# Kernel tuning notes

Hardware: AMD Instinct MI355X
Metric: run time of the kernel (lower is better)

## Reference

```python
import jax, jax.numpy as jnp
import numpy as np

N_EMBD = 1024
N_HEAD = 16
T_LEN = 4096
BATCH = 1


def setup_inputs() -> dict:
    key = jax.random.key(0)
    ks = jax.random.split(key, 9)
    C = N_EMBD
    s = 1.0 / np.sqrt(C)
    inp = {
        "x": jax.random.normal(ks[0], (BATCH, T_LEN, C), dtype=jnp.float32),
        "wq": jax.random.normal(ks[1], (C, C), dtype=jnp.float32) * s,
        "bq": jax.random.normal(ks[2], (C,), dtype=jnp.float32) * s,
        "wk": jax.random.normal(ks[3], (C, C), dtype=jnp.float32) * s,
        "bk": jax.random.normal(ks[4], (C,), dtype=jnp.float32) * s,
        "wv": jax.random.normal(ks[5], (C, C), dtype=jnp.float32) * s,
        "bv": jax.random.normal(ks[6], (C,), dtype=jnp.float32) * s,
        "wp": jax.random.normal(ks[7], (C, C), dtype=jnp.float32) * s,
        "bp": jax.random.normal(ks[8], (C,), dtype=jnp.float32) * s,
    }
    return inp


def reference(x, wq, bq, wk, bk, wv, bv, wp, bp):
    B, T, C = x.shape
    H = N_HEAD
    D = C // H  # head_dim
    # torch nn.Linear: y = x @ W.T + b
    def lin(x, w, b):
        return jnp.einsum("btc,oc->bto", x, w) + b
    q = lin(x, wq, bq).reshape(B, T, H, D).transpose(0, 2, 1, 3)  # bhtd
    k = lin(x, wk, bk).reshape(B, T, H, D).transpose(0, 2, 1, 3)
    v = lin(x, wv, bv).reshape(B, T, H, D).transpose(0, 2, 1, 3)
    att = jnp.einsum("bhqd,bhkd->bhqk", q, k) / jnp.sqrt(jnp.float32(D))
    causal = jnp.tril(jnp.ones((T, T), dtype=bool))  # [T,T]
    att = jnp.where(causal[None, None, :, :], att, -jnp.inf)
    att = jax.nn.softmax(att, axis=-1)
    # dropout p=0.0 -> identity (eval equivalent)
    y = jnp.einsum("bhqk,bhkd->bhqd", att, v)
    y = y.transpose(0, 2, 1, 3).reshape(B, T, C)
    return jnp.einsum("btc,oc->bto", y, wp) + bp
```

## Files before the change

kernel.cpp:

```cpp
#include <hip/hip_runtime.h>
#include <stdint.h>

#define T_LEN 4096
#define C_DIM 1024
#define NH 16
#define CLOG2E 0.18033688011112042f

typedef uint16_t u16;
typedef __attribute__((ext_vector_type(4))) float f32x4;
typedef __attribute__((ext_vector_type(8))) __bf16 bf16x8;
typedef __attribute__((ext_vector_type(8))) uint16_t u16x8;
typedef __attribute__((ext_vector_type(4))) float fvec4;

static __device__ __forceinline__ u16 f2b(float f) {
  union { float f; uint32_t u; } v; v.f = f;
  uint32_t u = v.u;
  return (u16)((u + 0x7fffu + ((u >> 16) & 1u)) >> 16);
}

static __device__ __forceinline__ float b2f(u16 b) {
  union { uint32_t u; float f; } v; v.u = ((uint32_t)b) << 16;
  return v.f;
}

static __device__ __forceinline__ uint32_t cvtpk(float lo, float hi) {
  uint32_t r;
  asm("v_cvt_pk_bf16_f32 %0, %1, %2" : "=v"(r) : "v"(lo), "v"(hi));
  return r;
}

static __device__ __forceinline__ f32x4 mfma16(u16x8 a, u16x8 b, f32x4 c) {
  return __builtin_amdgcn_mfma_f32_16x16x32_bf16(
      __builtin_bit_cast(bf16x8, a), __builtin_bit_cast(bf16x8, b), c, 0, 0, 0);
}

static __device__ __forceinline__ void gload_lds16(const void* g, void* l) {
  __builtin_amdgcn_global_load_lds(
      (const __attribute__((address_space(1))) uint32_t*)g,
      (__attribute__((address_space(3))) uint32_t*)l, 16, 0, 0);
}

__global__ void cast_all(const float* __restrict__ x,
                         const float* __restrict__ wq, const float* __restrict__ wk,
                         const float* __restrict__ wv, const float* __restrict__ wp,
                         u16* __restrict__ xb,
                         u16* __restrict__ wqb, u16* __restrict__ wkb,
                         u16* __restrict__ wvb, u16* __restrict__ wpb) {
  int i = blockIdx.x * blockDim.x + threadIdx.x;
  if (i >= 131072) return;
  const int z = blockIdx.y;
  const float* in;
  u16* out;
  if (z < 4) {
    in  = (z == 0) ? wq  : (z == 1) ? wk  : (z == 2) ? wv  : wp;
    out = (z == 0) ? wqb : (z == 1) ? wkb : (z == 2) ? wvb : wpb;
  } else {
    in  = x  + (size_t)(z - 4) * 131072 * 8;
    out = xb + (size_t)(z - 4) * 131072 * 8;
  }
  const fvec4* p = (const fvec4*)(in + (size_t)i * 8);
  fvec4 a = p[0], b = p[1];
  u16x8 o;
  o[0] = f2b(a[0]); o[1] = f2b(a[1]); o[2] = f2b(a[2]); o[3] = f2b(a[3]);
  o[4] = f2b(b[0]); o[5] = f2b(b[1]); o[6] = f2b(b[2]); o[7] = f2b(b[3]);
  *(u16x8*)(out + (size_t)i * 8) = o;
}

__global__ __launch_bounds__(256) void gemm_qkv(
    const u16* __restrict__ xb,
    const u16* __restrict__ wqb, const u16* __restrict__ wkb, const u16* __restrict__ wvb,
    const float* __restrict__ bq, const float* __restrict__ bk, const float* __restrict__ bv,
    u16* __restrict__ qh, u16* __restrict__ kh, u16* __restrict__ vt)
{
  __shared__ u16 sA[128 * 32];
  __shared__ u16 sB[128 * 32];
  const int K = C_DIM;
  const int z = blockIdx.z;
  const u16* wb = (z == 0) ? wqb : (z == 1) ? wkb : wvb;
  const float* bias = (z == 0) ? bq : (z == 1) ? bk : bv;
  const int m0 = blockIdx.x * 128;
  const int n0 = blockIdx.y * 128;
  const int tid = threadIdx.x;
  const int lane = tid & 63;
  const int w = tid >> 6;
  const int wm = (w >> 1) * 64;
  const int wn = (w & 1) * 64;
  const int lr = lane & 15;
  const int lk = (lane >> 4) * 8;

  f32x4 acc[4][4];
#pragma unroll
  for (int m = 0; m < 4; ++m)
#pragma unroll
    for (int n = 0; n < 4; ++n) acc[m][n] = (f32x4){0.f, 0.f, 0.f, 0.f};

  const int srow = tid >> 2;
  const int scol = (tid & 3) * 8;
  const u16* gA = xb + (size_t)(m0 + srow) * K + scol;
  const u16* gB = wb + (size_t)(n0 + srow) * K + scol;

  for (int k0 = 0; k0 < K; k0 += 32) {
    gload_lds16(gA + k0,          &sA[tid * 8]);
    gload_lds16(gA + 64 * K + k0, &sA[2048 + tid * 8]);
    gload_lds16(gB + k0,          &sB[tid * 8]);
    gload_lds16(gB + 64 * K + k0, &sB[2048 + tid * 8]);
    __syncthreads();
    u16x8 af[4], bfr[4];
#pragma unroll
    for (int m = 0; m < 4; ++m) af[m]  = *(const u16x8*)&sA[(wm + m * 16 + lr) * 32 + lk];
#pragma unroll
    for (int n = 0; n < 4; ++n) bfr[n] = *(const u16x8*)&sB[(wn + n * 16 + lr) * 32 + lk];
#pragma unroll
    for (int m = 0; m < 4; ++m)
#pragma unroll
      for (int n = 0; n < 4; ++n) acc[m][n] = mfma16(af[m], bfr[n], acc[m][n]);
    __syncthreads();
  }

  const int lg = lane >> 4;
#pragma unroll
  for (int n = 0; n < 4; ++n) {
    const int o = n0 + wn + n * 16 + lr;
    const float bb = bias[o];
    const int h = o >> 6;
    const int d = o & 63;
#pragma unroll
    for (int m = 0; m < 4; ++m) {
      const int tb = m0 + wm + m * 16 + lg * 4;
      if (z == 2) {
        uint2 pk;
        pk.x = cvtpk(acc[m][n][0] + bb, acc[m][n][1] + bb);
        pk.y = cvtpk(acc[m][n][2] + bb, acc[m][n][3] + bb);
        *(uint2*)&vt[(size_t)o * T_LEN + tb] = pk;
      } else if (z == 0) {
#pragma unroll
        for (int r = 0; r < 4; ++r)
          qh[((size_t)h * T_LEN + tb + r) * 64 + d] = f2b((acc[m][n][r] + bb) * CLOG2E);
      } else {
#pragma unroll
        for (int r = 0; r < 4; ++r)
          kh[((size_t)h * T_LEN + tb + r) * 64 + d] = f2b(acc[m][n][r] + bb);
      }
    }
  }
}

__global__ __launch_bounds__(256) void gemm_proj(
    const u16* __restrict__ yb, const u16* __restrict__ wpb,
    const float* __restrict__ bp, float* __restrict__ out)
{
  __shared__ u16 sA[128 * 32];
  __shared__ u16 sB[64 * 32];
  const int K = C_DIM;
  const int m0 = blockIdx.x * 128;
  const int n0 = blockIdx.y * 64;
  const int tid = threadIdx.x;
  const int lane = tid & 63;
  const int w = tid >> 6;
  const int wm = w * 32;
  const int lr = lane & 15;
  const int lk = (lane >> 4) * 8;

  f32x4 acc[2][4];
#pragma unroll
  for (int m = 0; m < 2; ++m)
#pragma unroll
    for (int n = 0; n < 4; ++n) acc[m][n] = (f32x4){0.f, 0.f, 0.f, 0.f};

  const int srow = tid >> 2;
  const int scol = (tid & 3) * 8;
  const u16* gA = yb  + (size_t)(m0 + srow) * K + scol;
  const u16* gB = wpb + (size_t)(n0 + srow) * K + scol;

  for (int k0 = 0; k0 < K; k0 += 32) {
    gload_lds16(gA + k0,          &sA[tid * 8]);
    gload_lds16(gA + 64 * K + k0, &sA[2048 + tid * 8]);
    gload_lds16(gB + k0,          &sB[tid * 8]);
    __syncthreads();
    u16x8 af[2], bfr[4];
#pragma unroll
    for (int m = 0; m < 2; ++m) af[m]  = *(const u16x8*)&sA[(wm + m * 16 + lr) * 32 + lk];
#pragma unroll
    for (int n = 0; n < 4; ++n) bfr[n] = *(const u16x8*)&sB[(n * 16 + lr) * 32 + lk];
#pragma unroll
    for (int m = 0; m < 2; ++m)
#pragma unroll
      for (int n = 0; n < 4; ++n) acc[m][n] = mfma16(af[m], bfr[n], acc[m][n]);
    __syncthreads();
  }

  const int lg = lane >> 4;
#pragma unroll
  for (int n = 0; n < 4; ++n) {
    const int o = n0 + n * 16 + lr;
    const float bb = bp[o];
#pragma unroll
    for (int m = 0; m < 2; ++m) {
      const int tb = m0 + wm + m * 16 + lg * 4;
#pragma unroll
      for (int r = 0; r < 4; ++r)
        out[(size_t)(tb + r) * C_DIM + o] = acc[m][n][r] + bb;
    }
  }
}

__global__ __launch_bounds__(256) void attn_kernel(
    const u16* __restrict__ qh, const u16* __restrict__ kh, const u16* __restrict__ vt,
    u16* __restrict__ y, u16* __restrict__ po, float* __restrict__ pml)
{
  __shared__ char skb[2][8192];
  __shared__ char svb[2][8192];
  __shared__ u16 pp[4][16][64];
  const int bid = blockIdx.x;
  const int j = bid >> 3;
  const int h = ((bid & 7) << 1) + (j & 1);
  const int i = j >> 1;
  int qb, c0;
  if (i < 32) { qb = 32 + i; c0 = 0; }
  else {
    const int k = (i - 32) >> 1;
    if (((i - 32) & 1) == 0) { qb = 63 - k; c0 = 1; }
    else                     { qb = 31 - k; c0 = -1; }
  }
  const int t0 = (c0 == 1) ? 32 : 0;
  const int t1 = (c0 == 0) ? 32 : (qb + 1);
  const bool hasdiag = (c0 != 0);

  const int tid = threadIdx.x;
  const int lane = tid & 63;
  const int w = tid >> 6;
  const int lr = lane & 15;
  const int lg = lane >> 4;
  const int sw = (lr & 7) << 4;
  const int qt0 = qb * 64 + w * 16;

  const int srow = tid >> 2;
  const int scb = (tid & 3) * 32;
  const int wo0 = srow * 128 + (scb ^ ((srow & 7) << 4));
  const int wo1 = srow * 128 + ((scb + 16) ^ ((srow & 7) << 4));
  const u16* gkbase = kh + ((size_t)h * T_LEN + srow) * 64 + (tid & 3) * 16;
  const u16* gvbase = vt + ((size_t)h * 64 + srow) * T_LEN + (tid & 3) * 16;
  char* ppb = (char*)&pp[w][0][0];

  const u16* qbase = qh + ((size_t)h * T_LEN + qt0 + lr) * 64 + lg * 8;
  u16x8 qf0 = *(const u16x8*)(qbase);
  u16x8 qf1 = *(const u16x8*)(qbase + 32);

  f32x4 oacc[4];
#pragma unroll
  for (int i2 = 0; i2 < 4; ++i2) oacc[i2] = (f32x4){0.f, 0.f, 0.f, 0.f};
  float mrow = -1e30f, lsum = 0.f;

  u16x8 ka = *(const u16x8*)(gkbase + (size_t)t0 * 4096);
  u16x8 kb = *(const u16x8*)(gkbase + (size_t)t0 * 4096 + 8);
  u16x8 va = *(const u16x8*)(gvbase + t0 * 64);
  u16x8 vb = *(const u16x8*)(gvbase + t0 * 64 + 8);
  *(u16x8*)(skb[0] + wo0) = ka; *(u16x8*)(skb[0] + wo1) = kb;
  *(u16x8*)(svb[0] + wo0) = va; *(u16x8*)(svb[0] + wo1) = vb;
  int cur = 0;

  for (int t = t0; t < t1; ++t) {
    __syncthreads();
    if (t + 1 < t1) {
      const size_t ko = (size_t)(t + 1) * 4096;
      ka = *(const u16x8*)(gkbase + ko);
      kb = *(const u16x8*)(gkbase + ko + 8);
      va = *(const u16x8*)(gvbase + (t + 1) * 64);
      vb = *(const u16x8*)(gvbase + (t + 1) * 64 + 8);
    }
    const char* skc = skb[cur];
    const char* svc = svb[cur];

    f32x4 sacc[4];
    __builtin_amdgcn_s_setprio(1);
#pragma unroll
    for (int i2 = 0; i2 < 4; ++i2) {
      const int ro = (i2 * 16 + lr) * 128;
      u16x8 a0 = *(const u16x8*)(skc + ro + ((lg * 16) ^ sw));
      u16x8 a1 = *(const u16x8*)(skc + ro + ((lg * 16 + 64) ^ sw));
      f32x4 zz = (f32x4){0.f, 0.f, 0.f, 0.f};
      zz = mfma16(a0, qf0, zz);
      zz = mfma16(a1, qf1, zz);
      sacc[i2] = zz;
    }
    __builtin_amdgcn_s_setprio(0);

    if (hasdiag && t == qb) {
      const int qg = qt0 + lr;
      const int kt0 = t * 64;
#pragma unroll
      for (int i2 = 0; i2 < 4; ++i2)
#pragma unroll
        for (int r = 0; r < 4; ++r) {
          const int kt = kt0 + i2 * 16 + lg * 4 + r;
          sacc[i2][r] = (kt <= qg) ? sacc[i2][r] : -1e30f;
        }
    }
    float x0 = fmaxf(fmaxf(sacc[0][0], sacc[0][1]), sacc[0][2]);
    float x1 = fmaxf(fmaxf(sacc[0][3], sacc[1][0]), sacc[1][1]);
    float x2 = fmaxf(fmaxf(sacc[1][2], sacc[1][3]), sacc[2][0]);
    float x3 = fmaxf(fmaxf(sacc[2][1], sacc[2][2]), sacc[2][3]);
    float x4 = fmaxf(fmaxf(sacc[3][0], sacc[3][1]), sacc[3][2]);
    float pm = fmaxf(fmaxf(fmaxf(x0, x1), fmaxf(x2, x3)), fmaxf(x4, sacc[3][3]));

    if (!__all(pm <= mrow)) {
      float pmf = fmaxf(pm, __shfl_xor(pm, 16));
      pmf = fmaxf(pmf, __shfl_xor(pmf, 32));
      const float mnew = fmaxf(mrow, pmf);
      const float sc = exp2f(mrow - mnew);
      lsum *= sc;
#pragma unroll
      for (int i2 = 0; i2 < 4; ++i2) oacc[i2] *= sc;
      mrow = mnew;
    }

    float u0 = 0.f, u1 = 0.f, u2 = 0.f, u3 = 0.f;
#pragma unroll
    for (int i2 = 0; i2 < 4; ++i2) {
      float e0 = exp2f(sacc[i2][0] - mrow);
      float e1 = exp2f(sacc[i2][1] - mrow);
      float e2 = exp2f(sacc[i2][2] - mrow);
      float e3 = exp2f(sacc[i2][3] - mrow);
      u0 += e0; u1 += e1; u2 += e2; u3 += e3;
      uint2 pk;
      pk.x = cvtpk(e0, e1);
      pk.y = cvtpk(e2, e3);
      *(uint2*)(ppb + ((lr * 128 + i2 * 32 + lg * 8) ^ sw)) = pk;
    }
    lsum += (u0 + u1) + (u2 + u3);

    __builtin_amdgcn_s_setprio(1);
#pragma unroll
    for (int ks = 0; ks < 2; ++ks) {
      u16x8 pf = *(const u16x8*)(ppb + ((lr * 128 + lg * 16 + ks * 64) ^ sw));
#pragma unroll
      for (int dblk = 0; dblk < 4; ++dblk) {
        const int ro = (dblk * 16 + lr) * 128;
        u16x8 vf = *(const u16x8*)(svc + ro + ((lg * 16 + ks * 64) ^ sw));
        oacc[dblk] = mfma16(vf, pf, oacc[dblk]);
      }
    }
    __builtin_amdgcn_s_setprio(0);

    if (t + 1 < t1) {
      char* dk = skb[cur ^ 1];
      char* dv = svb[cur ^ 1];
      *(u16x8*)(dk + wo0) = ka; *(u16x8*)(dk + wo1) = kb;
      *(u16x8*)(dv + wo0) = va; *(u16x8*)(dv + wo1) = vb;
    }
    cur ^= 1;
  }

  lsum += __shfl_xor(lsum, 16);
  lsum += __shfl_xor(lsum, 32);

  if (c0 < 0) {
    const float inv = 1.0f / lsum;
#pragma unroll
    for (int dblk = 0; dblk < 4; ++dblk) {
      uint2 pk;
      pk.x = cvtpk(oacc[dblk][0] * inv, oacc[dblk][1] * inv);
      pk.y = cvtpk(oacc[dblk][2] * inv, oacc[dblk][3] * inv);
      *(uint2*)&y[(size_t)(qt0 + lr) * C_DIM + h * 64 + dblk * 16 + lg * 4] = pk;
    }
  } else {
    const int slot = (((h << 5) + (qb - 32)) << 1) + c0;
    u16* pob = po + (size_t)slot * 4096 + (size_t)(w * 16 + lr) * 64;
#pragma unroll
    for (int dblk = 0; dblk < 4; ++dblk) {
      uint2 pk;
      pk.x = cvtpk(oacc[dblk][0], oacc[dblk][1]);
      pk.y = cvtpk(oacc[dblk][2], oacc[dblk][3]);
      *(uint2*)(pob + dblk * 16 + lg * 4) = pk;
    }
    if (lg == 0) {
      float2* pm2 = (float2*)pml;
      pm2[slot * 64 + w * 16 + lr] = make_float2(mrow, lsum);
    }
  }
}

__global__ __launch_bounds__(256) void attn_combine(
    const u16* __restrict__ po, const float* __restrict__ pml, u16* __restrict__ y)
{
  const int bid = blockIdx.x;
  const int h = bid >> 5;
  const int q5 = bid & 31;
  const int tid = threadIdx.x;
  const int row = tid >> 2;
  const int dseg = (tid & 3) * 16;
  const int slot0 = (((h << 5) + q5) << 1);
  const float2 ml0 = ((const float2*)pml)[slot0 * 64 + row];
  const float2 ml1 = ((const float2*)pml)[(slot0 + 1) * 64 + row];
  const float m = fmaxf(ml0.x, ml1.x);
  const float f0 = exp2f(ml0.x - m);
  const float f1 = exp2f(ml1.x - m);
  const float inv = 1.0f / (ml0.y * f0 + ml1.y * f1);
  const float g0 = f0 * inv, g1 = f1 * inv;
  const u16* p0 = po + (size_t)slot0 * 4096 + row * 64 + dseg;
  const u16* p1 = p0 + 4096;
  u16x8 a0 = *(const u16x8*)(p0);
  u16x8 a1 = *(const u16x8*)(p0 + 8);
  u16x8 b0 = *(const u16x8*)(p1);
  u16x8 b1 = *(const u16x8*)(p1 + 8);
  uint4 o0, o1;
  float r0, r1;
  r0 = b2f(a0[0]) * g0 + b2f(b0[0]) * g1; r1 = b2f(a0[1]) * g0 + b2f(b0[1]) * g1;
  o0.x = cvtpk(r0, r1);
  r0 = b2f(a0[2]) * g0 + b2f(b0[2]) * g1; r1 = b2f(a0[3]) * g0 + b2f(b0[3]) * g1;
  o0.y = cvtpk(r0, r1);
  r0 = b2f(a0[4]) * g0 + b2f(b0[4]) * g1; r1 = b2f(a0[5]) * g0 + b2f(b0[5]) * g1;
  o0.z = cvtpk(r0, r1);
  r0 = b2f(a0[6]) * g0 + b2f(b0[6]) * g1; r1 = b2f(a0[7]) * g0 + b2f(b0[7]) * g1;
  o0.w = cvtpk(r0, r1);
  r0 = b2f(a1[0]) * g0 + b2f(b1[0]) * g1; r1 = b2f(a1[1]) * g0 + b2f(b1[1]) * g1;
  o1.x = cvtpk(r0, r1);
  r0 = b2f(a1[2]) * g0 + b2f(b1[2]) * g1; r1 = b2f(a1[3]) * g0 + b2f(b1[3]) * g1;
  o1.y = cvtpk(r0, r1);
  r0 = b2f(a1[4]) * g0 + b2f(b1[4]) * g1; r1 = b2f(a1[5]) * g0 + b2f(b1[5]) * g1;
  o1.z = cvtpk(r0, r1);
  r0 = b2f(a1[6]) * g0 + b2f(b1[6]) * g1; r1 = b2f(a1[7]) * g0 + b2f(b1[7]) * g1;
  o1.w = cvtpk(r0, r1);
  u16* yp = y + (size_t)((q5 + 32) * 64 + row) * C_DIM + h * 64 + dseg;
  *(uint4*)(yp) = o0;
  *(uint4*)(yp + 8) = o1;
}

extern "C" void kernel_launch(void* const* d_in, const int* in_sizes, int n_in,
                              void* d_out, int out_size, void* d_ws, size_t ws_size,
                              hipStream_t stream) {
  const float* x  = (const float*)d_in[0];
  const float* wq = (const float*)d_in[1];
  const float* bq = (const float*)d_in[2];
  const float* wk = (const float*)d_in[3];
  const float* bk = (const float*)d_in[4];
  const float* wv = (const float*)d_in[5];
  const float* bv = (const float*)d_in[6];
  const float* wp = (const float*)d_in[7];
  const float* bp = (const float*)d_in[8];

  char* ws = (char*)d_ws;
  const size_t MB = 1024 * 1024;
  u16* xb  = (u16*)(ws + 0 * MB);
  u16* wqb = (u16*)(ws + 8 * MB);
  u16* wkb = (u16*)(ws + 10 * MB);
  u16* wvb = (u16*)(ws + 12 * MB);
  u16* wpb = (u16*)(ws + 14 * MB);
  u16* qh  = (u16*)(ws + 16 * MB);
  u16* kh  = (u16*)(ws + 24 * MB);
  u16* vt  = (u16*)(ws + 32 * MB);
  u16* y   = (u16*)(ws + 40 * MB);
  u16*   po  = (u16*)(ws + 0 * MB);
  float* pml = (float*)(ws + 8 * MB);

  cast_all<<<dim3(512, 8), dim3(256), 0, stream>>>(
      x, wq, wk, wv, wp, xb, wqb, wkb, wvb, wpb);

  gemm_qkv<<<dim3(32, 8, 3), dim3(256), 0, stream>>>(
      xb, wqb, wkb, wvb, bq, bk, bv, qh, kh, vt);

  attn_kernel<<<dim3(1536), dim3(256), 0, stream>>>(qh, kh, vt, y, po, pml);

  attn_combine<<<dim3(512), dim3(256), 0, stream>>>(po, pml, y);

  gemm_proj<<<dim3(32, 16), dim3(256), 0, stream>>>(y, wpb, bp, (float*)d_out);
}
```

Baseline: 144.1 us.

## Load K/V tiles directly into LDS and compute row sums via MFMA

Replaces the register-staged K/V prefetch (global load to VGPRs, then store to swizzled LDS after compute) with direct global-to-LDS loads into the next buffer, using a lane-swizzled column mapping. It also replaces the scalar exp-sum accumulation and end-of-loop shuffles with an extra MFMA against a ones vector, so the softmax denominator comes out of the matrix unit. This is meant to cut VGPR pressure, VALU work and LDS write instructions in the attention inner loop. The cost is one extra MFMA per k-step, and correctness now relies on the direct-to-LDS layout matching the existing swizzle and on the loads having completed before the barrier.

After: 145.0 us. About the same (+0.6%).

```diff
diff --git a/kernel.cpp b/kernel.cpp
--- a/kernel.cpp
+++ b/kernel.cpp
@@ -234,39 +234,50 @@
   const int sw = (lr & 7) << 4;
   const int qt0 = qb * 64 + w * 16;
 
-  const int srow = tid >> 2;
-  const int scb = (tid & 3) * 32;
-  const int wo0 = srow * 128 + (scb ^ ((srow & 7) << 4));
-  const int wo1 = srow * 128 + ((scb + 16) ^ ((srow & 7) << 4));
-  const u16* gkbase = kh + ((size_t)h * T_LEN + srow) * 64 + (tid & 3) * 16;
-  const u16* gvbase = vt + ((size_t)h * 64 + srow) * T_LEN + (tid & 3) * 16;
+  const int srl = lane >> 3;
+  const int col_el = ((lane & 7) ^ srl) * 8;
+  const int rowt = w * 16 + srl;
+  const u16* gks0 = kh + ((size_t)h * T_LEN + rowt) * 64 + col_el;
+  const u16* gks1 = gks0 + 8 * 64;
+  const u16* gvs0 = vt + ((size_t)h * 64 + rowt) * T_LEN + col_el;
+  const u16* gvs1 = gvs0 + 8 * T_LEN;
+  const int sd0 = w * 2048;
+  const int sd1 = sd0 + 1024;
   char* ppb = (char*)&pp[w][0][0];
 
   const u16* qbase = qh + ((size_t)h * T_LEN + qt0 + lr) * 64 + lg * 8;
   u16x8 qf0 = *(const u16x8*)(qbase);
   u16x8 qf1 = *(const u16x8*)(qbase + 32);
 
+  u16x8 ones;
+#pragma unroll
+  for (int r = 0; r < 8; ++r) ones[r] = 0x3F80;
+
   f32x4 oacc[4];
 #pragma unroll
   for (int i2 = 0; i2 < 4; ++i2) oacc[i2] = (f32x4){0.f, 0.f, 0.f, 0.f};
-  float mrow = -1e30f, lsum = 0.f;
-
-  u16x8 ka = *(const u16x8*)(gkbase + (size_t)t0 * 4096);
-  u16x8 kb = *(const u16x8*)(gkbase + (size_t)t0 * 4096 + 8);
-  u16x8 va = *(const u16x8*)(gvbase + t0 * 64);
-  u16x8 vb = *(const u16x8*)(gvbase + t0 * 64 + 8);
-  *(u16x8*)(skb[0] + wo0) = ka; *(u16x8*)(skb[0] + wo1) = kb;
-  *(u16x8*)(svb[0] + wo0) = va; *(u16x8*)(svb[0] + wo1) = vb;
+  f32x4 lacc = (f32x4){0.f, 0.f, 0.f, 0.f};
+  float mrow = -1e30f;
+
+  {
+    const size_t ko = (size_t)t0 * 4096;
+    const int vo = t0 * 64;
+    gload_lds16(gks0 + ko, skb[0] + sd0);
+    gload_lds16(gks1 + ko, skb[0] + sd1);
+    gload_lds16(gvs0 + vo, svb[0] + sd0);
+    gload_lds16(gvs1 + vo, svb[0] + sd1);
+  }
   int cur = 0;
 
   for (int t = t0; t < t1; ++t) {
     __syncthreads();
     if (t + 1 < t1) {
       const size_t ko = (size_t)(t + 1) * 4096;
-      ka = *(const u16x8*)(gkbase + ko);
-      kb = *(const u16x8*)(gkbase + ko + 8);
-      va = *(const u16x8*)(gvbase + (t + 1) * 64);
-      vb = *(const u16x8*)(gvbase + (t + 1) * 64 + 8);
+      const int vo = (t + 1) * 64;
+      gload_lds16(gks0 + ko, skb[cur ^ 1] + sd0);
+      gload_lds16(gks1 + ko, skb[cur ^ 1] + sd1);
+      gload_lds16(gvs0 + vo, svb[cur ^ 1] + sd0);
+      gload_lds16(gvs1 + vo, svb[cur ^ 1] + sd1);
     }
     const char* skc = skb[cur];
     const char* svc = svb[cur];
@@ -308,31 +319,29 @@
       pmf = fmaxf(pmf, __shfl_xor(pmf, 32));
       const float mnew = fmaxf(mrow, pmf);
       const float sc = exp2f(mrow - mnew);
-      lsum *= sc;
+      lacc *= sc;
 #pragma unroll
       for (int i2 = 0; i2 < 4; ++i2) oacc[i2] *= sc;
       mrow = mnew;
     }
 
-    float u0 = 0.f, u1 = 0.f, u2 = 0.f, u3 = 0.f;
 #pragma unroll
     for (int i2 = 0; i2 < 4; ++i2) {
       float e0 = exp2f(sacc[i2][0] - mrow);
       float e1 = exp2f(sacc[i2][1] - mrow);
       float e2 = exp2f(sacc[i2][2] - mrow);
       float e3 = exp2f(sacc[i2][3] - mrow);
-      u0 += e0; u1 += e1; u2 += e2; u3 += e3;
       uint2 pk;
       pk.x = cvtpk(e0, e1);
       pk.y = cvtpk(e2, e3);
       *(uint2*)(ppb + ((lr * 128 + i2 * 32 + lg * 8) ^ sw)) = pk;
     }
-    lsum += (u0 + u1) + (u2 + u3);
 
     __builtin_amdgcn_s_setprio(1);
 #pragma unroll
     for (int ks = 0; ks < 2; ++ks) {
       u16x8 pf = *(const u16x8*)(ppb + ((lr * 128 + lg * 16 + ks * 64) ^ sw));
+      lacc = mfma16(ones, pf, lacc);
 #pragma unroll
       for (int dblk = 0; dblk < 4; ++dblk) {
         const int ro = (dblk * 16 + lr) * 128;
@@ -342,17 +351,10 @@
     }
     __builtin_amdgcn_s_setprio(0);
 
-    if (t + 1 < t1) {
-      char* dk = skb[cur ^ 1];
-      char* dv = svb[cur ^ 1];
-      *(u16x8*)(dk + wo0) = ka; *(u16x8*)(dk + wo1) = kb;
-      *(u16x8*)(dv + wo0) = va; *(u16x8*)(dv + wo1) = vb;
-    }
     cur ^= 1;
   }
 
-  lsum += __shfl_xor(lsum, 16);
-  lsum += __shfl_xor(lsum, 32);
+  const float lsum = lacc[0];
 
   if (c0 < 0) {
     const float inv = 1.0f / lsum;
```

## Rebalance causal attention split into 28-tile KV chunks with three-way combine

Applied to the files above, without the earlier changes.

Replaces the old 32-tile split-KV scheme, where each block walks up to 32 KV tiles and the combine merges two partials, with a 28-tile chunking. Query blocks past 27 are split into two or three chunks, and the combine kernel merges up to three partials. The aim is to shorten the longest block's work so the 1728-block grid finishes with a smaller tail. It also drops the s_setprio hints around the MFMA sections and moves the pml buffer so it does not overlap the larger partial-output area. In exchange there are more blocks, more partial traffic and a slightly more complex combine step.

Measured after the change: 152.4 us. 1.06x slower.

```diff
diff --git a/kernel.cpp b/kernel.cpp
--- a/kernel.cpp
+++ b/kernel.cpp
@@ -215,16 +215,16 @@
   const int j = bid >> 3;
   const int h = ((bid & 7) << 1) + (j & 1);
   const int i = j >> 1;
-  int qb, c0;
-  if (i < 32) { qb = 32 + i; c0 = 0; }
-  else {
-    const int k = (i - 32) >> 1;
-    if (((i - 32) & 1) == 0) { qb = 63 - k; c0 = 1; }
-    else                     { qb = 31 - k; c0 = -1; }
-  }
-  const int t0 = (c0 == 1) ? 32 : 0;
-  const int t1 = (c0 == 0) ? 32 : (qb + 1);
-  const bool hasdiag = (c0 != 0);
+  int qb, c;
+  if (i < 36)       { qb = 28 + i;          c = 0; }
+  else if (i < 44)  { qb = 56 + (i - 36);   c = 1; }
+  else if (i < 72)  { qb = 27 - (i - 44);   c = 0; }
+  else if (i < 100) { qb = 55 - (i - 72);   c = 1; }
+  else              { qb = 63 - (i - 100);  c = 2; }
+  const int t0 = c * 28;
+  const int t1e = 28 * (c + 1);
+  const int t1 = (t1e < qb + 1) ? t1e : (qb + 1);
+  const bool direct = (qb <= 27);
 
   const int tid = threadIdx.x;
   const int lane = tid & 63;
@@ -272,7 +272,6 @@
     const char* svc = svb[cur];
 
     f32x4 sacc[4];
-    __builtin_amdgcn_s_setprio(1);
 #pragma unroll
     for (int i2 = 0; i2 < 4; ++i2) {
       const int ro = (i2 * 16 + lr) * 128;
@@ -283,9 +282,8 @@
       zz = mfma16(a1, qf1, zz);
       sacc[i2] = zz;
     }
-    __builtin_amdgcn_s_setprio(0);
-
-    if (hasdiag && t == qb) {
+
+    if (t == qb) {
       const int qg = qt0 + lr;
       const int kt0 = t * 64;
 #pragma unroll
@@ -329,7 +327,6 @@
     }
     lsum += (u0 + u1) + (u2 + u3);
 
-    __builtin_amdgcn_s_setprio(1);
 #pragma unroll
     for (int ks = 0; ks < 2; ++ks) {
       u16x8 pf = *(const u16x8*)(ppb + ((lr * 128 + lg * 16 + ks * 64) ^ sw));
@@ -340,7 +337,6 @@
         oacc[dblk] = mfma16(vf, pf, oacc[dblk]);
       }
     }
-    __builtin_amdgcn_s_setprio(0);
 
     if (t + 1 < t1) {
       char* dk = skb[cur ^ 1];
@@ -354,7 +350,7 @@
   lsum += __shfl_xor(lsum, 16);
   lsum += __shfl_xor(lsum, 32);
 
-  if (c0 < 0) {
+  if (direct) {
     const float inv = 1.0f / lsum;
 #pragma unroll
     for (int dblk = 0; dblk < 4; ++dblk) {
@@ -364,7 +360,8 @@
       *(uint2*)&y[(size_t)(qt0 + lr) * C_DIM + h * 64 + dblk * 16 + lg * 4] = pk;
     }
   } else {
-    const int slot = (((h << 5) + (qb - 32)) << 1) + c0;
+    const int sb = (qb <= 55) ? (qb - 28) * 2 : 56 + (qb - 56) * 3;
+    const int slot = h * 80 + sb + c;
     u16* pob = po + (size_t)slot * 4096 + (size_t)(w * 16 + lr) * 64;
 #pragma unroll
     for (int dblk = 0; dblk < 4; ++dblk) {
@@ -384,44 +381,48 @@
     const u16* __restrict__ po, const float* __restrict__ pml, u16* __restrict__ y)
 {
   const int bid = blockIdx.x;
-  const int h = bid >> 5;
-  const int q5 = bid & 31;
+  const int h = bid / 36;
+  const int qi = bid - h * 36;
+  const int qb = 28 + qi;
+  const int nch = (qb <= 55) ? 2 : 3;
+  const int sb = (qb <= 55) ? (qb - 28) * 2 : 56 + (qb - 56) * 3;
+  const int slot0 = h * 80 + sb;
   const int tid = threadIdx.x;
   const int row = tid >> 2;
   const int dseg = (tid & 3) * 16;
-  const int slot0 = (((h << 5) + q5) << 1);
-  const float2 ml0 = ((const float2*)pml)[slot0 * 64 + row];
-  const float2 ml1 = ((const float2*)pml)[(slot0 + 1) * 64 + row];
-  const float m = fmaxf(ml0.x, ml1.x);
+  const float2* pm2 = (const float2*)pml;
+
+  float2 ml0 = pm2[(slot0 + 0) * 64 + row];
+  float2 ml1 = pm2[(slot0 + 1) * 64 + row];
+  float2 ml2 = make_float2(-1e30f, 0.f);
+  float m = fmaxf(ml0.x, ml1.x);
+  if (nch == 3) { ml2 = pm2[(slot0 + 2) * 64 + row]; m = fmaxf(m, ml2.x); }
   const float f0 = exp2f(ml0.x - m);
   const float f1 = exp2f(ml1.x - m);
-  const float inv = 1.0f / (ml0.y * f0 + ml1.y * f1);
-  const float g0 = f0 * inv, g1 = f1 * inv;
-  const u16* p0 = po + (size_t)slot0 * 4096 + row * 64 + dseg;
-  const u16* p1 = p0 + 4096;
-  u16x8 a0 = *(const u16x8*)(p0);
-  u16x8 a1 = *(const u16x8*)(p0 + 8);
-  u16x8 b0 = *(const u16x8*)(p1);
-  u16x8 b1 = *(const u16x8*)(p1 + 8);
+  const float f2 = (nch == 3) ? exp2f(ml2.x - m) : 0.f;
+  const float L = ml0.y * f0 + ml1.y * f1 + ml2.y * f2;
+  const float inv = 1.0f / L;
+  const float g0 = f0 * inv, g1 = f1 * inv, g2 = f2 * inv;
+
+  float acc[16];
+#pragma unroll
+  for (int e = 0; e < 16; ++e) acc[e] = 0.f;
+  for (int cc = 0; cc < nch; ++cc) {
+    const float g = (cc == 0) ? g0 : (cc == 1) ? g1 : g2;
+    const u16* p = po + (size_t)(slot0 + cc) * 4096 + row * 64 + dseg;
+    u16x8 a0 = *(const u16x8*)(p);
+    u16x8 a1 = *(const u16x8*)(p + 8);
+#pragma unroll
+    for (int e = 0; e < 8; ++e) acc[e]     += b2f(a0[e]) * g;
+#pragma unroll
+    for (int e = 0; e < 8; ++e) acc[8 + e] += b2f(a1[e]) * g;
+  }
   uint4 o0, o1;
-  float r0, r1;
-  r0 = b2f(a0[0]) * g0 + b2f(b0[0]) * g1; r1 = b2f(a0[1]) * g0 + b2f(b0[1]) * g1;
-  o0.x = cvtpk(r0, r1);
-  r0 = b2f(a0[2]) * g0 + b2f(b0[2]) * g1; r1 = b2f(a0[3]) * g0 + b2f(b0[3]) * g1;
-  o0.y = cvtpk(r0, r1);
-  r0 = b2f(a0[4]) * g0 + b2f(b0[4]) * g1; r1 = b2f(a0[5]) * g0 + b2f(b0[5]) * g1;
-  o0.z = cvtpk(r0, r1);
-  r0 = b2f(a0[6]) * g0 + b2f(b0[6]) * g1; r1 = b2f(a0[7]) * g0 + b2f(b0[7]) * g1;
-  o0.w = cvtpk(r0, r1);
-  r0 = b2f(a1[0]) * g0 + b2f(b1[0]) * g1; r1 = b2f(a1[1]) * g0 + b2f(b1[1]) * g1;
-  o1.x = cvtpk(r0, r1);
-  r0 = b2f(a1[2]) * g0 + b2f(b1[2]) * g1; r1 = b2f(a1[3]) * g0 + b2f(b1[3]) * g1;
-  o1.y = cvtpk(r0, r1);
-  r0 = b2f(a1[4]) * g0 + b2f(b1[4]) * g1; r1 = b2f(a1[5]) * g0 + b2f(b1[5]) * g1;
-  o1.z = cvtpk(r0, r1);
-  r0 = b2f(a1[6]) * g0 + b2f(b1[6]) * g1; r1 = b2f(a1[7]) * g0 + b2f(b1[7]) * g1;
-  o1.w = cvtpk(r0, r1);
-  u16* yp = y + (size_t)((q5 + 32) * 64 + row) * C_DIM + h * 64 + dseg;
+  o0.x = cvtpk(acc[0], acc[1]);   o0.y = cvtpk(acc[2], acc[3]);
+  o0.z = cvtpk(acc[4], acc[5]);   o0.w = cvtpk(acc[6], acc[7]);
+  o1.x = cvtpk(acc[8], acc[9]);   o1.y = cvtpk(acc[10], acc[11]);
+  o1.z = cvtpk(acc[12], acc[13]); o1.w = cvtpk(acc[14], acc[15]);
+  u16* yp = y + (size_t)(qb * 64 + row) * C_DIM + h * 64 + dseg;
   *(uint4*)(yp) = o0;
   *(uint4*)(yp + 8) = o1;
 }
@@ -451,7 +452,7 @@
   u16* vt  = (u16*)(ws + 32 * MB);
   u16* y   = (u16*)(ws + 40 * MB);
   u16*   po  = (u16*)(ws + 0 * MB);
-  float* pml = (float*)(ws + 8 * MB);
+  float* pml = (float*)(ws + 11 * MB);
 
   cast_all<<<dim3(512, 8), dim3(256), 0, stream>>>(
       x, wq, wk, wv, wp, xb, wqb, wkb, wvb, wpb);
@@ -459,9 +460,9 @@
   gemm_qkv<<<dim3(32, 8, 3), dim3(256), 0, stream>>>(
       xb, wqb, wkb, wvb, bq, bk, bv, qh, kh, vt);
 
-  attn_kernel<<<dim3(1536), dim3(256), 0, stream>>>(qh, kh, vt, y, po, pml);
-
-  attn_combine<<<dim3(512), dim3(256), 0, stream>>>(po, pml, y);
+  attn_kernel<<<dim3(1728), dim3(256), 0, stream>>>(qh, kh, vt, y, po, pml);
+
+  attn_combine<<<dim3(576), dim3(256), 0, stream>>>(po, pml, y);
 
   gemm_proj<<<dim3(32, 16), dim3(256), 0, stream>>>(y, wpb, bp, (float*)d_out);
 }
```
